# Optimization experiments

Measured on AMD Instinct MI355X. Metric: run time of the kernel, lower is better.

The kernel has to match this reference:

```python
import jax, jax.numpy as jnp
import numpy as np

B, T, I, H = 4096, 120, 64, 128


def setup_inputs() -> dict:
    key = jax.random.key(0)
    ks = jax.random.split(key, 5)
    s = 1.0 / np.sqrt(H)
    return {
        "x": jax.random.normal(ks[0], (B, T, I), dtype=jnp.float32),
        "W_ih": jax.random.uniform(ks[1], (3 * H, I), jnp.float32, -s, s),
        "W_hh": jax.random.uniform(ks[2], (3 * H, H), jnp.float32, -s, s),
        "b_ih": jax.random.uniform(ks[3], (3 * H,), jnp.float32, -s, s),
        "b_hh": jax.random.uniform(ks[4], (3 * H,), jnp.float32, -s, s),
    }


def reference(x, W_ih, W_hh, b_ih, b_hh):
    # x: [B, T, I]; PyTorch GRUCell gate order: reset, update, new.
    Bv, Tv, _ = x.shape
    Hv = W_hh.shape[1]
    # Precompute input-side gate projections for all timesteps (same math,
    # hoisted out of the recurrence): [B, T, 3H]
    x_gates = jnp.einsum("bti,gi->btg", x, W_ih) + b_ih

    def step(h, xg_t):
        hg = h @ W_hh.T + b_hh  # [B, 3H]
        xr, xz, xn = jnp.split(xg_t, 3, axis=-1)
        hr, hz, hn = jnp.split(hg, 3, axis=-1)
        r = jax.nn.sigmoid(xr + hr)
        z = jax.nn.sigmoid(xz + hz)
        n = jnp.tanh(xn + r * hn)
        h_new = (1.0 - z) * n + z * h
        return h_new, h_new

    h0 = jnp.zeros((Bv, Hv), dtype=x.dtype)
    h_T, outs = jax.lax.scan(step, h0, jnp.swapaxes(x_gates, 0, 1))  # outs: [T, B, H]
    outputs = jnp.swapaxes(outs, 0, 1)  # [B, T, H]
    return outputs, h_T
```

## Files before the change

kernel.cpp:

```cpp
#include <hip/hip_runtime.h>


#define Bv 4096
#define Tv 120
#define Iv 64
#define Hv 128

typedef __attribute__((ext_vector_type(8))) short short8;
typedef __attribute__((ext_vector_type(4))) float floatx4;
typedef __attribute__((ext_vector_type(2))) unsigned uintx2;

#if __has_builtin(__builtin_amdgcn_exp2f)
#define EXP2F(x) __builtin_amdgcn_exp2f(x)
#else
#define EXP2F(x) exp2f(x)
#endif
#if __has_builtin(__builtin_amdgcn_rcpf)
#define RCPF(x) __builtin_amdgcn_rcpf(x)
#else
#define RCPF(x) (1.0f / (x))
#endif

__device__ inline short f2bf(float f) {
    union { float f; unsigned u; } v; v.f = f;
    unsigned r = v.u + 0x7FFFu + ((v.u >> 16) & 1u);
    return (short)(r >> 16);
}

__device__ inline unsigned cvt_pk_bf16(float a, float b) {
    unsigned d;
    asm("v_cvt_pk_bf16_f32 %0, %1, %2" : "=v"(d) : "v"(a), "v"(b));
    return d;
}

__device__ inline float sigmoid_fast(float x) {
    return RCPF(1.0f + EXP2F(-1.44269504f * x));
}
__device__ inline float tanh_fast(float x) {
    return 1.0f - 2.0f * RCPF(1.0f + EXP2F(2.88539008f * x));
}

__device__ inline void lds_barrier() {
    asm volatile("s_waitcnt lgkmcnt(0)" ::: "memory");
    __builtin_amdgcn_s_barrier();
    asm volatile("" ::: "memory");
    __builtin_amdgcn_sched_barrier(0);
}

__launch_bounds__(512, 2)
__global__ void gru_persist(const float* __restrict__ x,
                            const float* __restrict__ W_ih,
                            const float* __restrict__ W_hh,
                            const float* __restrict__ b_ih,
                            const float* __restrict__ b_hh,
                            float* __restrict__ out) {
    constexpr int XSTR = 72;
    constexpr int HSTR = 136;
    __shared__ short h_lds[16 * HSTR];
    __shared__ short x_lds[2][16 * XSTR];

    const int tid  = threadIdx.x;
    const int wave = tid >> 6;
    const int lane = tid & 63;
    const int s    = lane & 15;
    const int quad = lane >> 4;
    const int b0   = blockIdx.x * 16;
    const int c    = wave * 16 + s;
    const int cb   = wave * 16 + quad * 4;

    floatx4 bias_r  = *(const floatx4*)(b_ih + cb)       + *(const floatx4*)(b_hh + cb);
    floatx4 bias_z  = *(const floatx4*)(b_ih + 128 + cb) + *(const floatx4*)(b_hh + 128 + cb);
    floatx4 bias_xn = *(const floatx4*)(b_ih + 256 + cb);
    floatx4 bias_hn = *(const floatx4*)(b_hh + 256 + cb);

    short8 whh[3][4];
    short8 wih[3][2];
#pragma unroll
    for (int g = 0; g < 3; ++g) {
        const float* wr = W_hh + (size_t)(g * 128 + c) * 128;
#pragma unroll
        for (int kst = 0; kst < 4; ++kst) {
            const float* p = wr + kst * 32 + quad * 8;
            floatx4 lo = *(const floatx4*)p;
            floatx4 hi = *(const floatx4*)(p + 4);
            short8 f;
            f[0] = f2bf(lo[0]); f[1] = f2bf(lo[1]); f[2] = f2bf(lo[2]); f[3] = f2bf(lo[3]);
            f[4] = f2bf(hi[0]); f[5] = f2bf(hi[1]); f[6] = f2bf(hi[2]); f[7] = f2bf(hi[3]);
            whh[g][kst] = f;
        }
        const float* wi = W_ih + (size_t)(g * 128 + c) * 64;
#pragma unroll
        for (int kst = 0; kst < 2; ++kst) {
            const float* p = wi + kst * 32 + quad * 8;
            floatx4 lo = *(const floatx4*)p;
            floatx4 hi = *(const floatx4*)(p + 4);
            short8 f;
            f[0] = f2bf(lo[0]); f[1] = f2bf(lo[1]); f[2] = f2bf(lo[2]); f[3] = f2bf(lo[3]);
            f[4] = f2bf(hi[0]); f[5] = f2bf(hi[1]); f[6] = f2bf(hi[2]); f[7] = f2bf(hi[3]);
            wih[g][kst] = f;
        }
    }

    for (int i = tid; i < 16 * HSTR; i += 512) h_lds[i] = 0;
    floatx4 hcar = {0.f, 0.f, 0.f, 0.f};

    const int xrow = tid >> 5, xcp = tid & 31;
    const float* xbase = x + ((size_t)(b0 + xrow) * Tv) * Iv + xcp * 2;
    {
        float2 v = *(const float2*)xbase;
        *(unsigned*)&x_lds[0][xrow * XSTR + xcp * 2] = cvt_pk_bf16(v.x, v.y);
    }
    float2 xv_cur = *(const float2*)(xbase + (size_t)1 * Iv);
    __syncthreads();

    float* optr = out + ((size_t)(b0 + s) * Tv) * Hv + cb;
    float* hT   = out + (size_t)Bv * Tv * Hv;

#pragma unroll 1
    for (int t = 0; t < Tv; ++t) {
        float2 xv_next = {0.f, 0.f};
        if (t + 2 < Tv) xv_next = *(const float2*)(xbase + (size_t)(t + 2) * Iv);

        const short* hrow = &h_lds[s * HSTR];
        short8 ah0 = *(const short8*)(hrow + quad * 8);
        short8 ah1 = *(const short8*)(hrow + 32 + quad * 8);
        short8 ah2 = *(const short8*)(hrow + 64 + quad * 8);
        short8 ah3 = *(const short8*)(hrow + 96 + quad * 8);
        const short* xr = &x_lds[t & 1][s * XSTR];
        short8 ax0 = *(const short8*)(xr + quad * 8);
        short8 ax1 = *(const short8*)(xr + 32 + quad * 8);

        floatx4 accr  = __builtin_amdgcn_mfma_f32_16x16x32_bf16(whh[0][0], ah0, bias_r, 0, 0, 0);
        floatx4 accz  = __builtin_amdgcn_mfma_f32_16x16x32_bf16(whh[1][0], ah0, bias_z, 0, 0, 0);
        floatx4 acchn = __builtin_amdgcn_mfma_f32_16x16x32_bf16(whh[2][0], ah0, bias_hn, 0, 0, 0);
        accr  = __builtin_amdgcn_mfma_f32_16x16x32_bf16(whh[0][1], ah1, accr, 0, 0, 0);
        accz  = __builtin_amdgcn_mfma_f32_16x16x32_bf16(whh[1][1], ah1, accz, 0, 0, 0);
        acchn = __builtin_amdgcn_mfma_f32_16x16x32_bf16(whh[2][1], ah1, acchn, 0, 0, 0);
        accr  = __builtin_amdgcn_mfma_f32_16x16x32_bf16(whh[0][2], ah2, accr, 0, 0, 0);
        accz  = __builtin_amdgcn_mfma_f32_16x16x32_bf16(whh[1][2], ah2, accz, 0, 0, 0);
        acchn = __builtin_amdgcn_mfma_f32_16x16x32_bf16(whh[2][2], ah2, acchn, 0, 0, 0);
        accr  = __builtin_amdgcn_mfma_f32_16x16x32_bf16(whh[0][3], ah3, accr, 0, 0, 0);
        accz  = __builtin_amdgcn_mfma_f32_16x16x32_bf16(whh[1][3], ah3, accz, 0, 0, 0);
        acchn = __builtin_amdgcn_mfma_f32_16x16x32_bf16(whh[2][3], ah3, acchn, 0, 0, 0);

        floatx4 accxn = __builtin_amdgcn_mfma_f32_16x16x32_bf16(wih[2][0], ax0, bias_xn, 0, 0, 0);
        accr  = __builtin_amdgcn_mfma_f32_16x16x32_bf16(wih[0][0], ax0, accr, 0, 0, 0);
        accz  = __builtin_amdgcn_mfma_f32_16x16x32_bf16(wih[1][0], ax0, accz, 0, 0, 0);
        accxn = __builtin_amdgcn_mfma_f32_16x16x32_bf16(wih[2][1], ax1, accxn, 0, 0, 0);
        accr  = __builtin_amdgcn_mfma_f32_16x16x32_bf16(wih[0][1], ax1, accr, 0, 0, 0);
        accz  = __builtin_amdgcn_mfma_f32_16x16x32_bf16(wih[1][1], ax1, accz, 0, 0, 0);

        lds_barrier();

        floatx4 hv;
#pragma unroll
        for (int r = 0; r < 4; ++r) {
            float rg = sigmoid_fast(accr[r]);
            float zg = sigmoid_fast(accz[r]);
            float ng = tanh_fast(fmaf(rg, acchn[r], accxn[r]));
            float h  = fmaf(zg, hcar[r] - ng, ng);
            hcar[r] = h;
            hv[r]   = h;
        }

        uintx2 hp;
        hp[0] = cvt_pk_bf16(hv[0], hv[1]);
        hp[1] = cvt_pk_bf16(hv[2], hv[3]);
        *(uintx2*)&h_lds[s * HSTR + cb] = hp;

        if (t + 1 < Tv) {
            *(unsigned*)&x_lds[(t + 1) & 1][xrow * XSTR + xcp * 2] =
                cvt_pk_bf16(xv_cur.x, xv_cur.y);
        }
        xv_cur = xv_next;

        *(floatx4*)optr = hv;
        optr += Hv;

        lds_barrier();
    }

    *(floatx4*)(hT + (size_t)(b0 + s) * Hv + cb) = hcar;
}

extern "C" void kernel_launch(void* const* d_in, const int* in_sizes, int n_in,
                              void* d_out, int out_size, void* d_ws, size_t ws_size,
                              hipStream_t stream) {
    (void)in_sizes; (void)n_in; (void)out_size; (void)d_ws; (void)ws_size;
    const float* x    = (const float*)d_in[0];
    const float* W_ih = (const float*)d_in[1];
    const float* W_hh = (const float*)d_in[2];
    const float* b_ih = (const float*)d_in[3];
    const float* b_hh = (const float*)d_in[4];
    float* out = (float*)d_out;
    hipLaunchKernelGGL(gru_persist, dim3(Bv / 16), dim3(512), 0, stream,
                       x, W_ih, W_hh, b_ih, b_hh, out);
}
```

Measured before the change: 420.2 us.

## Precompute next-step input projection off the recurrent critical path

```diff
diff --git a/kernel.cpp b/kernel.cpp
--- a/kernel.cpp
+++ b/kernel.cpp
@@ -38,13 +38,6 @@
 }
 __device__ inline float tanh_fast(float x) {
     return 1.0f - 2.0f * RCPF(1.0f + EXP2F(2.88539008f * x));
-}
-
-__device__ inline void lds_barrier() {
-    asm volatile("s_waitcnt lgkmcnt(0)" ::: "memory");
-    __builtin_amdgcn_s_barrier();
-    asm volatile("" ::: "memory");
-    __builtin_amdgcn_sched_barrier(0);
 }
 
 __launch_bounds__(512, 2)
@@ -113,6 +106,19 @@
     float2 xv_cur = *(const float2*)(xbase + (size_t)1 * Iv);
     __syncthreads();
 
+    floatx4 xpr, xpz, xpxn;
+    {
+        const short* xr = &x_lds[0][s * XSTR];
+        short8 ax0 = *(const short8*)(xr + quad * 8);
+        short8 ax1 = *(const short8*)(xr + 32 + quad * 8);
+        xpr  = __builtin_amdgcn_mfma_f32_16x16x32_bf16(wih[0][0], ax0, bias_r, 0, 0, 0);
+        xpz  = __builtin_amdgcn_mfma_f32_16x16x32_bf16(wih[1][0], ax0, bias_z, 0, 0, 0);
+        xpxn = __builtin_amdgcn_mfma_f32_16x16x32_bf16(wih[2][0], ax0, bias_xn, 0, 0, 0);
+        xpr  = __builtin_amdgcn_mfma_f32_16x16x32_bf16(wih[0][1], ax1, xpr, 0, 0, 0);
+        xpz  = __builtin_amdgcn_mfma_f32_16x16x32_bf16(wih[1][1], ax1, xpz, 0, 0, 0);
+        xpxn = __builtin_amdgcn_mfma_f32_16x16x32_bf16(wih[2][1], ax1, xpxn, 0, 0, 0);
+    }
+
     float* optr = out + ((size_t)(b0 + s) * Tv) * Hv + cb;
     float* hT   = out + (size_t)Bv * Tv * Hv;
 
@@ -126,12 +132,9 @@
         short8 ah1 = *(const short8*)(hrow + 32 + quad * 8);
         short8 ah2 = *(const short8*)(hrow + 64 + quad * 8);
         short8 ah3 = *(const short8*)(hrow + 96 + quad * 8);
-        const short* xr = &x_lds[t & 1][s * XSTR];
-        short8 ax0 = *(const short8*)(xr + quad * 8);
-        short8 ax1 = *(const short8*)(xr + 32 + quad * 8);
-
-        floatx4 accr  = __builtin_amdgcn_mfma_f32_16x16x32_bf16(whh[0][0], ah0, bias_r, 0, 0, 0);
-        floatx4 accz  = __builtin_amdgcn_mfma_f32_16x16x32_bf16(whh[1][0], ah0, bias_z, 0, 0, 0);
+
+        floatx4 accr  = __builtin_amdgcn_mfma_f32_16x16x32_bf16(whh[0][0], ah0, xpr, 0, 0, 0);
+        floatx4 accz  = __builtin_amdgcn_mfma_f32_16x16x32_bf16(whh[1][0], ah0, xpz, 0, 0, 0);
         floatx4 acchn = __builtin_amdgcn_mfma_f32_16x16x32_bf16(whh[2][0], ah0, bias_hn, 0, 0, 0);
         accr  = __builtin_amdgcn_mfma_f32_16x16x32_bf16(whh[0][1], ah1, accr, 0, 0, 0);
         accz  = __builtin_amdgcn_mfma_f32_16x16x32_bf16(whh[1][1], ah1, accz, 0, 0, 0);
@@ -143,21 +146,20 @@
         accz  = __builtin_amdgcn_mfma_f32_16x16x32_bf16(whh[1][3], ah3, accz, 0, 0, 0);
         acchn = __builtin_amdgcn_mfma_f32_16x16x32_bf16(whh[2][3], ah3, acchn, 0, 0, 0);
 
-        floatx4 accxn = __builtin_amdgcn_mfma_f32_16x16x32_bf16(wih[2][0], ax0, bias_xn, 0, 0, 0);
-        accr  = __builtin_amdgcn_mfma_f32_16x16x32_bf16(wih[0][0], ax0, accr, 0, 0, 0);
-        accz  = __builtin_amdgcn_mfma_f32_16x16x32_bf16(wih[1][0], ax0, accz, 0, 0, 0);
-        accxn = __builtin_amdgcn_mfma_f32_16x16x32_bf16(wih[2][1], ax1, accxn, 0, 0, 0);
-        accr  = __builtin_amdgcn_mfma_f32_16x16x32_bf16(wih[0][1], ax1, accr, 0, 0, 0);
-        accz  = __builtin_amdgcn_mfma_f32_16x16x32_bf16(wih[1][1], ax1, accz, 0, 0, 0);
-
-        lds_barrier();
+        if (t + 1 < Tv) {
+            *(unsigned*)&x_lds[(t + 1) & 1][xrow * XSTR + xcp * 2] =
+                cvt_pk_bf16(xv_cur.x, xv_cur.y);
+        }
+        xv_cur = xv_next;
+
+        __syncthreads();
 
         floatx4 hv;
 #pragma unroll
         for (int r = 0; r < 4; ++r) {
             float rg = sigmoid_fast(accr[r]);
             float zg = sigmoid_fast(accz[r]);
-            float ng = tanh_fast(fmaf(rg, acchn[r], accxn[r]));
+            float ng = tanh_fast(fmaf(rg, acchn[r], xpxn[r]));
             float h  = fmaf(zg, hcar[r] - ng, ng);
             hcar[r] = h;
             hv[r]   = h;
@@ -168,16 +170,22 @@
         hp[1] = cvt_pk_bf16(hv[2], hv[3]);
         *(uintx2*)&h_lds[s * HSTR + cb] = hp;
 
-        if (t + 1 < Tv) {
-            *(unsigned*)&x_lds[(t + 1) & 1][xrow * XSTR + xcp * 2] =
-                cvt_pk_bf16(xv_cur.x, xv_cur.y);
-        }
-        xv_cur = xv_next;
-
         *(floatx4*)optr = hv;
         optr += Hv;
 
-        lds_barrier();
+        if (t + 1 < Tv) {
+            const short* xr = &x_lds[(t + 1) & 1][s * XSTR];
+            short8 ax0 = *(const short8*)(xr + quad * 8);
+            short8 ax1 = *(const short8*)(xr + 32 + quad * 8);
+            xpr  = __builtin_amdgcn_mfma_f32_16x16x32_bf16(wih[0][0], ax0, bias_r, 0, 0, 0);
+            xpz  = __builtin_amdgcn_mfma_f32_16x16x32_bf16(wih[1][0], ax0, bias_z, 0, 0, 0);
+            xpxn = __builtin_amdgcn_mfma_f32_16x16x32_bf16(wih[2][0], ax0, bias_xn, 0, 0, 0);
+            xpr  = __builtin_amdgcn_mfma_f32_16x16x32_bf16(wih[0][1], ax1, xpr, 0, 0, 0);
+            xpz  = __builtin_amdgcn_mfma_f32_16x16x32_bf16(wih[1][1], ax1, xpz, 0, 0, 0);
+            xpxn = __builtin_amdgcn_mfma_f32_16x16x32_bf16(wih[2][1], ax1, xpxn, 0, 0, 0);
+        }
+
+        __syncthreads();
     }
 
     *(floatx4*)(hT + (size_t)(b0 + s) * Hv + cb) = hcar;
```

Result: slower. 449.5 us (+7.0%).
